# Kernel tuning notes

Measured on AMD Instinct MI355X. Metric: run time of the kernel, lower is better.

Reference implementation:

```python
import jax, jax.numpy as jnp
import numpy as np

EMBED_DIM = 1024
NUM_HEADS = 16
HEAD_DIM = EMBED_DIM // NUM_HEADS
B, S = 2, 2048


def setup_inputs() -> dict:
    key = jax.random.key(0)
    ks = jax.random.split(key, 11)
    scale = 1.0 / np.sqrt(EMBED_DIM)
    inp = {
        "q": jax.random.normal(ks[0], (B, S, EMBED_DIM), jnp.float32),
        "k": jax.random.normal(ks[1], (B, S, EMBED_DIM), jnp.float32),
        "v": jax.random.normal(ks[2], (B, S, EMBED_DIM), jnp.float32),
        "Wq": jax.random.normal(ks[3], (EMBED_DIM, EMBED_DIM), jnp.float32) * scale,
        "bq": jnp.zeros((EMBED_DIM,), jnp.float32),
        "Wk": jax.random.normal(ks[4], (EMBED_DIM, EMBED_DIM), jnp.float32) * scale,
        "bk": jnp.zeros((EMBED_DIM,), jnp.float32),
        "Wv": jax.random.normal(ks[5], (EMBED_DIM, EMBED_DIM), jnp.float32) * scale,
        "bv": jnp.zeros((EMBED_DIM,), jnp.float32),
        "Wo": jax.random.normal(ks[6], (EMBED_DIM, EMBED_DIM), jnp.float32) * scale,
        "bo": jnp.zeros((EMBED_DIM,), jnp.float32),
    }
    return inp


def _split_heads(x):
    # [B, S, E] -> [B, H, S, D]
    b, s, _ = x.shape
    return x.reshape(b, s, NUM_HEADS, HEAD_DIM).transpose(0, 2, 1, 3)


def reference(q, k, v, Wq, bq, Wk, bk, Wv, bv, Wo, bo):
    query = _split_heads(q @ Wq + bq)  # [B,H,S,D]
    key_ = _split_heads(k @ Wk + bk)
    value = _split_heads(v @ Wv + bv)
    # scaled dot-product attention (scale by sqrt(head_dim), as in source)
    logits = jnp.einsum("bhqd,bhkd->bhqk", query, key_) / jnp.sqrt(
        jnp.asarray(HEAD_DIM, jnp.float32)
    )
    weights = jax.nn.softmax(logits, axis=-1)
    attn = jnp.einsum("bhqk,bhkd->bhqd", weights, value)  # [B,H,S,D]
    concat = attn.transpose(0, 2, 1, 3).reshape(q.shape[0], -1, EMBED_DIM)
    return concat @ Wo + bo
```

## Files before the change

kernel.cpp:

```cpp
#include <hip/hip_runtime.h>
#include <hip/hip_bf16.h>
#include <math.h>


typedef short bf16x8 __attribute__((ext_vector_type(8)));
typedef short bf16x4 __attribute__((ext_vector_type(4)));
typedef float f32x4 __attribute__((ext_vector_type(4)));
typedef unsigned short u16;
typedef unsigned int u32;

#if defined(__HIP_DEVICE_COMPILE__) && __has_builtin(__builtin_amdgcn_mfma_f32_16x16x16_bf16)
#define MFMA16(a, b, c) __builtin_amdgcn_mfma_f32_16x16x16_bf16(a, b, c, 0, 0, 0)
#else
#define MFMA16(a, b, c) __builtin_amdgcn_mfma_f32_16x16x16bf16_1k(a, b, c, 0, 0, 0)
#endif

#define QSCALE 0.18033688011112042f

__device__ __forceinline__ u16 f2b(float f) {
  union { float f; unsigned u; } v; v.f = f;
  unsigned r = v.u + 0x7FFF + ((v.u >> 16) & 1);
  return (u16)(r >> 16);
}

__device__ __forceinline__ void glds16(const u16* g, u16* l) {
  __builtin_amdgcn_global_load_lds(
      (const __attribute__((address_space(1))) u32*)g,
      (__attribute__((address_space(3))) u32*)l, 16, 0, 0);
}

__global__ void prep(const float* __restrict__ q, const float* __restrict__ k,
                     const float* __restrict__ v, u16* __restrict__ qo,
                     u16* __restrict__ ko, u16* __restrict__ vo,
                     const float* __restrict__ W0, const float* __restrict__ W1,
                     const float* __restrict__ W2, const float* __restrict__ W3,
                     u16* __restrict__ T0, u16* __restrict__ T1,
                     u16* __restrict__ T2, u16* __restrict__ T3) {
  __shared__ float tile[64][65];
  int z = blockIdx.y;
  if (z < 3) {
    const float* in = z == 0 ? q : (z == 1 ? k : v);
    u16* out = z == 0 ? qo : (z == 1 ? ko : vo);
    int i = (blockIdx.x * 256 + threadIdx.x) * 8;
    float4 a = *(const float4*)(in + i);
    float4 b = *(const float4*)(in + i + 4);
    union { u16 u[8]; uint4 v4; } o;
    o.u[0] = f2b(a.x); o.u[1] = f2b(a.y); o.u[2] = f2b(a.z); o.u[3] = f2b(a.w);
    o.u[4] = f2b(b.x); o.u[5] = f2b(b.y); o.u[6] = f2b(b.z); o.u[7] = f2b(b.w);
    *(uint4*)(out + i) = o.v4;
  } else {
    int bx = blockIdx.x;
    if (bx >= 1024) return;
    int wsel = bx >> 8, tid2 = bx & 255;
    const float* W = wsel == 0 ? W0 : (wsel == 1 ? W1 : (wsel == 2 ? W2 : W3));
    u16* WT = wsel == 0 ? T0 : (wsel == 1 ? T1 : (wsel == 2 ? T2 : T3));
    int k0 = (tid2 >> 4) * 64, n0 = (tid2 & 15) * 64;
    int c = threadIdx.x & 63, r0 = threadIdx.x >> 6;
    #pragma unroll
    for (int i = 0; i < 64; i += 4)
      tile[r0 + i][c] = W[(k0 + r0 + i) * 1024 + n0 + c];
    __syncthreads();
    #pragma unroll
    for (int i = 0; i < 64; i += 4)
      WT[(n0 + r0 + i) * 1024 + k0 + c] = f2b(tile[c][r0 + i]);
  }
}

template<int MODE, int BN>
__device__ __forceinline__ void gemm_core(
    const u16* __restrict__ A, const u16* __restrict__ BT,
    const float* __restrict__ bias, void* __restrict__ out,
    int bx, int by, float scale) {
  constexpr int NT = BN / 64 * 2;
  __shared__ u16 As[128 * 64];
  __shared__ u16 Bs[BN * 64];
  const int tid = threadIdx.x;
  const int w = tid >> 6, lane = tid & 63;
  const int wm = w >> 1, wn = w & 1;
  const int q = lane >> 4, l16 = lane & 15;
  const int m0 = by * 128, n0 = bx * BN;
  const int K = 1024;

  f32x4 acc[4][NT] = {};
  for (int k0 = 0; k0 < K; k0 += 64) {
    __syncthreads();
    #pragma unroll
    for (int p = 0; p < 4; ++p) {
      int c = p * 4 + w;
      int ci = c * 64 + lane;
      int r = ci >> 3, b = ci & 7;
      glds16(A + (m0 + r) * K + k0 + ((b ^ (r & 7)) * 8), As + c * 512);
    }
    #pragma unroll
    for (int p = 0; p < BN / 32; ++p) {
      int c = p * 4 + w;
      int ci = c * 64 + lane;
      int r = ci >> 3, b = ci & 7;
      glds16(BT + (n0 + r) * K + k0 + ((b ^ (r & 7)) * 8), Bs + c * 512);
    }
    __builtin_amdgcn_s_waitcnt(0xF70);
    __syncthreads();
    #pragma unroll
    for (int ks = 0; ks < 2; ++ks) {
      bf16x8 af[4], bf[NT];
      #pragma unroll
      for (int mt = 0; mt < 4; ++mt) {
        int row = wm * 64 + mt * 16 + l16;
        af[mt] = *(const bf16x8*)(As + row * 64 + (((ks * 4 + q) ^ (row & 7)) * 8));
      }
      #pragma unroll
      for (int nt = 0; nt < NT; ++nt) {
        int row = wn * (BN / 2) + nt * 16 + l16;
        bf[nt] = *(const bf16x8*)(Bs + row * 64 + (((ks * 4 + q) ^ (row & 7)) * 8));
      }
      #pragma unroll
      for (int mt = 0; mt < 4; ++mt)
        #pragma unroll
        for (int nt = 0; nt < NT; ++nt)
          acc[mt][nt] = __builtin_amdgcn_mfma_f32_16x16x32_bf16(af[mt], bf[nt], acc[mt][nt], 0, 0, 0);
    }
  }
  #pragma unroll
  for (int mt = 0; mt < 4; ++mt)
    #pragma unroll
    for (int nt = 0; nt < NT; ++nt) {
      int col = n0 + wn * (BN / 2) + nt * 16 + l16;
      float bcol = bias[col];
      if (MODE == 2) {
        int rbase = m0 + wm * 64 + mt * 16 + q * 4;
        int b = rbase >> 11, s0 = rbase & 2047;
        int h = col >> 6, d = col & 63;
        union { u16 u[4]; uint2 v; } o;
        #pragma unroll
        for (int reg = 0; reg < 4; ++reg)
          o.u[reg] = f2b(acc[mt][nt][reg] + bcol);
        *(uint2*)((u16*)out + (((b << 4) + h) * 64 + d) * 2048 + s0) = o.v;
      } else {
        #pragma unroll
        for (int reg = 0; reg < 4; ++reg) {
          int row = m0 + wm * 64 + mt * 16 + q * 4 + reg;
          float val = (acc[mt][nt][reg] + bcol) * scale;
          if (MODE == 0) {
            int b = row >> 11, s = row & 2047, h = col >> 6, d = col & 63;
            ((u16*)out)[(((b << 4) + h) * 2048 + s) * 64 + d] = f2b(val);
          } else {
            ((float*)out)[row * 1024 + col] = val;
          }
        }
      }
    }
}

__global__ __launch_bounds__(256) void gemm_qkv(
    const u16* qb, const u16* kb, const u16* vb,
    const u16* WqT, const u16* WkT, const u16* WvT,
    const float* bq, const float* bk, const float* bv,
    u16* Qh, u16* Kh, u16* VhT) {
  int z = blockIdx.z;
  if (z == 0)      gemm_core<0, 128>(qb, WqT, bq, Qh,  blockIdx.x, blockIdx.y, QSCALE);
  else if (z == 1) gemm_core<0, 128>(kb, WkT, bk, Kh,  blockIdx.x, blockIdx.y, 1.0f);
  else             gemm_core<2, 128>(vb, WvT, bv, VhT, blockIdx.x, blockIdx.y, 1.0f);
}

__global__ __launch_bounds__(256) void gemm_out(
    const u16* A, const u16* BT, const float* bias, float* out) {
  gemm_core<1, 64>(A, BT, bias, out, blockIdx.x, blockIdx.y, 1.0f);
}

__global__ __launch_bounds__(512, 4) void flash_attn(
    const u16* __restrict__ Qh, const u16* __restrict__ Kh,
    const u16* __restrict__ VTh, u16* __restrict__ Oo) {
  __shared__ __align__(16) u16 smem[32768];
  const int tid = threadIdx.x, w = tid >> 6, lane = tid & 63;
  const int g = w >> 2, w4 = w & 3;
  const int q = lane >> 4, l16 = lane & 15;
  const int bh = blockIdx.x & 31, qt = blockIdx.x >> 5;
  const u16* Qp = Qh + (bh * 2048 + qt * 128) * 64;
  const u16* Kp = Kh + (bh * 2048 + g * 1024) * 64;
  const u16* Vp = VTh + bh * 64 * 2048 + g * 1024;
  u16* Ksg = smem + g * 8192;
  u16* Vtg = smem + 16384 + g * 8192;

  bf16x8 aq[2][2];
  #pragma unroll
  for (int rb = 0; rb < 2; ++rb)
    #pragma unroll
    for (int ks = 0; ks < 2; ++ks)
      aq[rb][ks] = *(const bf16x8*)(Qp + (w4 * 32 + rb * 16 + l16) * 64 + ks * 32 + q * 8);

  const int sr = (lane & 7) ^ (lane >> 3);
  auto stage = [&](int kt, int buf) {
    #pragma unroll
    for (int p = 0; p < 2; ++p) {
      int c = p * 4 + w4;
      int r = c * 8 + (lane >> 3);
      glds16(Kp + (kt * 64 + r) * 64 + sr * 8, Ksg + buf * 4096 + c * 512);
    }
    #pragma unroll
    for (int p = 0; p < 2; ++p) {
      int c = p * 4 + w4;
      int r = c * 8 + (lane >> 3);
      glds16(Vp + r * 2048 + kt * 64 + sr * 8, Vtg + buf * 4096 + c * 512);
    }
  };
  stage(0, 0);

  f32x4 oacc[4][2] = {};
  float lacc[2] = {0.f, 0.f};

  for (int kt = 0; kt < 16; ++kt) {
    const int buf = kt & 1;
    __builtin_amdgcn_s_waitcnt(0xF70);
    __syncthreads();
    if (kt + 1 < 16) stage(kt + 1, buf ^ 1);

    const u16* KsT = Ksg + buf * 4096;
    const u16* VtT = Vtg + buf * 4096;

    f32x4 st[2][4] = {};
    __builtin_amdgcn_s_setprio(1);
    #pragma unroll
    for (int ks = 0; ks < 2; ++ks) {
      bf16x8 bk[4];
      #pragma unroll
      for (int nt = 0; nt < 4; ++nt) {
        int row = nt * 16 + l16;
        bk[nt] = *(const bf16x8*)(KsT + row * 64 + (((ks * 4 + q) ^ (l16 & 7)) * 8));
      }
      #pragma unroll
      for (int rb = 0; rb < 2; ++rb)
        #pragma unroll
        for (int nt = 0; nt < 4; ++nt)
          st[rb][nt] = __builtin_amdgcn_mfma_f32_16x16x32_bf16(bk[nt], aq[rb][ks], st[rb][nt], 0, 0, 0);
    }
    __builtin_amdgcn_s_setprio(0);

    #pragma unroll
    for (int rb = 0; rb < 2; ++rb)
      #pragma unroll
      for (int nt = 0; nt < 4; ++nt)
        #pragma unroll
        for (int reg = 0; reg < 4; ++reg) {
          float p = __builtin_amdgcn_exp2f(st[rb][nt][reg]);
          lacc[rb] += p;
          st[rb][nt][reg] = p;
        }

    __builtin_amdgcn_s_setprio(1);
    #pragma unroll
    for (int kb = 0; kb < 4; ++kb) {
      bf16x4 pf[2];
      #pragma unroll
      for (int rb = 0; rb < 2; ++rb) {
        union { u32 u[2]; bf16x4 v; } pk;
        pk.u[0] = __builtin_amdgcn_perm(__float_as_uint(st[rb][kb][1]),
                                        __float_as_uint(st[rb][kb][0]), 0x07060302u);
        pk.u[1] = __builtin_amdgcn_perm(__float_as_uint(st[rb][kb][3]),
                                        __float_as_uint(st[rb][kb][2]), 0x07060302u);
        pf[rb] = pk.v;
      }
      #pragma unroll
      for (int ntd = 0; ntd < 4; ++ntd) {
        int row = ntd * 16 + l16;
        int c = kb * 2 + (q >> 1);
        bf16x4 vf = *(const bf16x4*)(VtT + row * 64 + ((c ^ (l16 & 7)) * 8) + (q & 1) * 4);
        #pragma unroll
        for (int rb = 0; rb < 2; ++rb)
          oacc[ntd][rb] = MFMA16(vf, pf[rb], oacc[ntd][rb]);
      }
    }
    __builtin_amdgcn_s_setprio(0);
  }

  __syncthreads();
  float* Ocmb = (float*)smem;
  float* Lcmb = (float*)(smem + 18432);
  const int idx = w4 * 64 + lane;
  if (g == 1) {
    #pragma unroll
    for (int ntd = 0; ntd < 4; ++ntd)
      #pragma unroll
      for (int rb = 0; rb < 2; ++rb)
        *(f32x4*)(Ocmb + idx * 36 + ntd * 8 + rb * 4) = oacc[ntd][rb];
    Lcmb[idx * 2 + 0] = lacc[0];
    Lcmb[idx * 2 + 1] = lacc[1];
  }
  __syncthreads();
  if (g == 0) {
    #pragma unroll
    for (int ntd = 0; ntd < 4; ++ntd)
      #pragma unroll
      for (int rb = 0; rb < 2; ++rb)
        oacc[ntd][rb] += *(const f32x4*)(Ocmb + idx * 36 + ntd * 8 + rb * 4);
    lacc[0] += Lcmb[idx * 2 + 0];
    lacc[1] += Lcmb[idx * 2 + 1];

    const int b = bh >> 4, h = bh & 15;
    #pragma unroll
    for (int rb = 0; rb < 2; ++rb) {
      float s = lacc[rb];
      s += __shfl_xor(s, 16);
      s += __shfl_xor(s, 32);
      float rl = 0.998046875f / s;
      int row = b * 2048 + qt * 128 + w4 * 32 + rb * 16 + l16;
      #pragma unroll
      for (int ntd = 0; ntd < 4; ++ntd) {
        union { u16 u[4]; uint2 v; } o;
        #pragma unroll
        for (int reg = 0; reg < 4; ++reg)
          o.u[reg] = f2b(oacc[ntd][rb][reg] * rl);
        *(uint2*)(Oo + row * 1024 + h * 64 + ntd * 16 + q * 4) = o.v;
      }
    }
  }
}

extern "C" void kernel_launch(void* const* d_in, const int* in_sizes, int n_in,
                              void* d_out, int out_size, void* d_ws, size_t ws_size,
                              hipStream_t stream) {
  const float* q  = (const float*)d_in[0];
  const float* k  = (const float*)d_in[1];
  const float* v  = (const float*)d_in[2];
  const float* Wq = (const float*)d_in[3];
  const float* bq = (const float*)d_in[4];
  const float* Wk = (const float*)d_in[5];
  const float* bk = (const float*)d_in[6];
  const float* Wv = (const float*)d_in[7];
  const float* bv = (const float*)d_in[8];
  const float* Wo = (const float*)d_in[9];
  const float* bo = (const float*)d_in[10];

  char* ws = (char*)d_ws;
  const size_t MB = 1024 * 1024;
  u16* qb  = (u16*)(ws);
  u16* kb  = (u16*)(ws + 8 * MB);
  u16* vb  = (u16*)(ws + 16 * MB);
  u16* WqT = (u16*)(ws + 24 * MB);
  u16* WkT = (u16*)(ws + 26 * MB);
  u16* WvT = (u16*)(ws + 28 * MB);
  u16* WoT = (u16*)(ws + 30 * MB);
  u16* Qh  = (u16*)(ws + 32 * MB);
  u16* Kh  = (u16*)(ws + 40 * MB);
  u16* VhT = (u16*)(ws + 48 * MB);
  u16* Ao  = (u16*)(ws + 56 * MB);

  prep<<<dim3(2048, 4), 256, 0, stream>>>(q, k, v, qb, kb, vb,
                                          Wq, Wk, Wv, Wo, WqT, WkT, WvT, WoT);
  gemm_qkv<<<dim3(8, 32, 3), 256, 0, stream>>>(qb, kb, vb, WqT, WkT, WvT,
                                               bq, bk, bv, Qh, Kh, VhT);
  flash_attn<<<512, 512, 0, stream>>>(Qh, Kh, VhT, Ao);
  gemm_out<<<dim3(16, 32), 256, 0, stream>>>(Ao, WoT, bo, (float*)d_out);
}
```

Before: 227.6 us.

## Drop split-KV in flash attention, use 4-wave blocks, widen output GEMM tile

The flash attention kernel stops splitting the key range across two wave groups. Each 256-thread block now walks all 32 key tiles itself, which removes the shared-memory cross-group reduction and its extra barriers, and halves LDS use so more blocks can fit per CU. The exp/row-sum loop is rewritten as a tree-style partial sum, and the output GEMM moves to a 128-wide tile with half as many blocks. In exchange, each wave has a longer serial loop with less parallelism per block, and the output GEMM grid is smaller.

Result: slower. 291.8 us (+28.2%).

```diff
diff --git a/kernel.cpp b/kernel.cpp
--- a/kernel.cpp
+++ b/kernel.cpp
@@ -164,43 +164,42 @@
 
 __global__ __launch_bounds__(256) void gemm_out(
     const u16* A, const u16* BT, const float* bias, float* out) {
-  gemm_core<1, 64>(A, BT, bias, out, blockIdx.x, blockIdx.y, 1.0f);
-}
-
-__global__ __launch_bounds__(512, 4) void flash_attn(
+  gemm_core<1, 128>(A, BT, bias, out, blockIdx.x, blockIdx.y, 1.0f);
+}
+
+__global__ __launch_bounds__(256, 5) void flash_attn(
     const u16* __restrict__ Qh, const u16* __restrict__ Kh,
     const u16* __restrict__ VTh, u16* __restrict__ Oo) {
-  __shared__ __align__(16) u16 smem[32768];
+  __shared__ __align__(16) u16 Ks[2][4096];
+  __shared__ __align__(16) u16 Vt[2][4096];
+
   const int tid = threadIdx.x, w = tid >> 6, lane = tid & 63;
-  const int g = w >> 2, w4 = w & 3;
   const int q = lane >> 4, l16 = lane & 15;
   const int bh = blockIdx.x & 31, qt = blockIdx.x >> 5;
   const u16* Qp = Qh + (bh * 2048 + qt * 128) * 64;
-  const u16* Kp = Kh + (bh * 2048 + g * 1024) * 64;
-  const u16* Vp = VTh + bh * 64 * 2048 + g * 1024;
-  u16* Ksg = smem + g * 8192;
-  u16* Vtg = smem + 16384 + g * 8192;
+  const u16* Kp = Kh + bh * 2048 * 64;
+  const u16* Vp = VTh + bh * 64 * 2048;
 
   bf16x8 aq[2][2];
   #pragma unroll
   for (int rb = 0; rb < 2; ++rb)
     #pragma unroll
     for (int ks = 0; ks < 2; ++ks)
-      aq[rb][ks] = *(const bf16x8*)(Qp + (w4 * 32 + rb * 16 + l16) * 64 + ks * 32 + q * 8);
+      aq[rb][ks] = *(const bf16x8*)(Qp + (w * 32 + rb * 16 + l16) * 64 + ks * 32 + q * 8);
 
   const int sr = (lane & 7) ^ (lane >> 3);
   auto stage = [&](int kt, int buf) {
     #pragma unroll
     for (int p = 0; p < 2; ++p) {
-      int c = p * 4 + w4;
+      int c = p * 4 + w;
       int r = c * 8 + (lane >> 3);
-      glds16(Kp + (kt * 64 + r) * 64 + sr * 8, Ksg + buf * 4096 + c * 512);
+      glds16(Kp + (kt * 64 + r) * 64 + sr * 8, &Ks[buf][c * 512]);
     }
     #pragma unroll
     for (int p = 0; p < 2; ++p) {
-      int c = p * 4 + w4;
+      int c = p * 4 + w;
       int r = c * 8 + (lane >> 3);
-      glds16(Vp + r * 2048 + kt * 64 + sr * 8, Vtg + buf * 4096 + c * 512);
+      glds16(Vp + r * 2048 + kt * 64 + sr * 8, &Vt[buf][c * 512]);
     }
   };
   stage(0, 0);
@@ -208,14 +207,14 @@
   f32x4 oacc[4][2] = {};
   float lacc[2] = {0.f, 0.f};
 
-  for (int kt = 0; kt < 16; ++kt) {
+  for (int kt = 0; kt < 32; ++kt) {
     const int buf = kt & 1;
     __builtin_amdgcn_s_waitcnt(0xF70);
     __syncthreads();
-    if (kt + 1 < 16) stage(kt + 1, buf ^ 1);
-
-    const u16* KsT = Ksg + buf * 4096;
-    const u16* VtT = Vtg + buf * 4096;
+    if (kt + 1 < 32) stage(kt + 1, buf ^ 1);
+
+    const u16* KsT = Ks[buf];
+    const u16* VtT = Vt[buf];
 
     f32x4 st[2][4] = {};
     __builtin_amdgcn_s_setprio(1);
@@ -236,15 +235,20 @@
     __builtin_amdgcn_s_setprio(0);
 
     #pragma unroll
-    for (int rb = 0; rb < 2; ++rb)
-      #pragma unroll
-      for (int nt = 0; nt < 4; ++nt)
-        #pragma unroll
-        for (int reg = 0; reg < 4; ++reg) {
-          float p = __builtin_amdgcn_exp2f(st[rb][nt][reg]);
-          lacc[rb] += p;
-          st[rb][nt][reg] = p;
-        }
+    for (int rb = 0; rb < 2; ++rb) {
+      float part[4];
+      #pragma unroll
+      for (int nt = 0; nt < 4; ++nt) {
+        float p0 = __builtin_amdgcn_exp2f(st[rb][nt][0]);
+        float p1 = __builtin_amdgcn_exp2f(st[rb][nt][1]);
+        float p2 = __builtin_amdgcn_exp2f(st[rb][nt][2]);
+        float p3 = __builtin_amdgcn_exp2f(st[rb][nt][3]);
+        st[rb][nt][0] = p0; st[rb][nt][1] = p1;
+        st[rb][nt][2] = p2; st[rb][nt][3] = p3;
+        part[nt] = (p0 + p1) + (p2 + p3);
+      }
+      lacc[rb] += (part[0] + part[1]) + (part[2] + part[3]);
+    }
 
     __builtin_amdgcn_s_setprio(1);
     #pragma unroll
@@ -272,45 +276,26 @@
     __builtin_amdgcn_s_setprio(0);
   }
 
-  __syncthreads();
-  float* Ocmb = (float*)smem;
-  float* Lcmb = (float*)(smem + 18432);
-  const int idx = w4 * 64 + lane;
-  if (g == 1) {
-    #pragma unroll
-    for (int ntd = 0; ntd < 4; ++ntd)
-      #pragma unroll
-      for (int rb = 0; rb < 2; ++rb)
-        *(f32x4*)(Ocmb + idx * 36 + ntd * 8 + rb * 4) = oacc[ntd][rb];
-    Lcmb[idx * 2 + 0] = lacc[0];
-    Lcmb[idx * 2 + 1] = lacc[1];
-  }
-  __syncthreads();
-  if (g == 0) {
-    #pragma unroll
-    for (int ntd = 0; ntd < 4; ++ntd)
-      #pragma unroll
-      for (int rb = 0; rb < 2; ++rb)
-        oacc[ntd][rb] += *(const f32x4*)(Ocmb + idx * 36 + ntd * 8 + rb * 4);
-    lacc[0] += Lcmb[idx * 2 + 0];
-    lacc[1] += Lcmb[idx * 2 + 1];
-
-    const int b = bh >> 4, h = bh & 15;
-    #pragma unroll
-    for (int rb = 0; rb < 2; ++rb) {
-      float s = lacc[rb];
-      s += __shfl_xor(s, 16);
-      s += __shfl_xor(s, 32);
-      float rl = 0.998046875f / s;
-      int row = b * 2048 + qt * 128 + w4 * 32 + rb * 16 + l16;
-      #pragma unroll
-      for (int ntd = 0; ntd < 4; ++ntd) {
-        union { u16 u[4]; uint2 v; } o;
-        #pragma unroll
-        for (int reg = 0; reg < 4; ++reg)
-          o.u[reg] = f2b(oacc[ntd][rb][reg] * rl);
-        *(uint2*)(Oo + row * 1024 + h * 64 + ntd * 16 + q * 4) = o.v;
-      }
+  float rl[2];
+  #pragma unroll
+  for (int rb = 0; rb < 2; ++rb) {
+    float s = lacc[rb];
+    s += __shfl_xor(s, 16);
+    s += __shfl_xor(s, 32);
+    rl[rb] = 0.998046875f / s;
+  }
+
+  const int b = bh >> 4, h = bh & 15;
+  #pragma unroll
+  for (int rb = 0; rb < 2; ++rb) {
+    int row = b * 2048 + qt * 128 + w * 32 + rb * 16 + l16;
+    #pragma unroll
+    for (int ntd = 0; ntd < 4; ++ntd) {
+      union { u16 u[4]; uint2 v; } o;
+      #pragma unroll
+      for (int reg = 0; reg < 4; ++reg)
+        o.u[reg] = f2b(oacc[ntd][rb][reg] * rl[rb]);
+      *(uint2*)(Oo + row * 1024 + h * 64 + ntd * 16 + q * 4) = o.v;
     }
   }
 }
@@ -348,6 +333,6 @@
                                           Wq, Wk, Wv, Wo, WqT, WkT, WvT, WoT);
   gemm_qkv<<<dim3(8, 32, 3), 256, 0, stream>>>(qb, kb, vb, WqT, WkT, WvT,
                                                bq, bk, bv, Qh, Kh, VhT);
-  flash_attn<<<512, 512, 0, stream>>>(Qh, Kh, VhT, Ao);
-  gemm_out<<<dim3(16, 32), 256, 0, stream>>>(Ao, WoT, bo, (float*)d_out);
-}
+  flash_attn<<<512, 256, 0, stream>>>(Qh, Kh, VhT, Ao);
+  gemm_out<<<dim3(8, 32), 256, 0, stream>>>(Ao, WoT, bo, (float*)d_out);
+}
```

## Fuse fp32-to-bf16 input conversion into QKV projection GEMM tile loads

Applied to the files above, without the earlier changes.

Removes the separate pass that converted q/k/v activations to bf16, and has the QKV GEMM load fp32 tiles directly into LDS with a swizzled layout. Each fragment is converted to bf16 with packed convert instructions just before the MFMAs. This avoids writing and re-reading the bf16 copies of the activations, at the cost of double LDS for the A tile, twice the global bytes per A tile load, and extra conversion instructions in the inner loop. The weight transpose becomes its own kernel.

New measurement: 265.2 us. 1.16x slower.

```diff
diff --git a/kernel.cpp b/kernel.cpp
--- a/kernel.cpp
+++ b/kernel.cpp
@@ -23,57 +23,53 @@
   return (u16)(r >> 16);
 }
 
+__device__ __forceinline__ u32 cvtpk2(float a, float b) {
+  u32 r;
+#if defined(__HIP_DEVICE_COMPILE__)
+  asm("v_cvt_pk_bf16_f32 %0, %1, %2" : "=v"(r) : "v"(a), "v"(b));
+#else
+  r = ((u32)f2b(b) << 16) | f2b(a);
+#endif
+  return r;
+}
+
 __device__ __forceinline__ void glds16(const u16* g, u16* l) {
   __builtin_amdgcn_global_load_lds(
       (const __attribute__((address_space(1))) u32*)g,
       (__attribute__((address_space(3))) u32*)l, 16, 0, 0);
 }
-
-__global__ void prep(const float* __restrict__ q, const float* __restrict__ k,
-                     const float* __restrict__ v, u16* __restrict__ qo,
-                     u16* __restrict__ ko, u16* __restrict__ vo,
-                     const float* __restrict__ W0, const float* __restrict__ W1,
-                     const float* __restrict__ W2, const float* __restrict__ W3,
-                     u16* __restrict__ T0, u16* __restrict__ T1,
-                     u16* __restrict__ T2, u16* __restrict__ T3) {
+__device__ __forceinline__ void glds16f(const float* g, float* l) {
+  __builtin_amdgcn_global_load_lds(
+      (const __attribute__((address_space(1))) u32*)g,
+      (__attribute__((address_space(3))) u32*)l, 16, 0, 0);
+}
+
+__global__ void transpose_w4(const float* __restrict__ W0, const float* __restrict__ W1,
+                             const float* __restrict__ W2, const float* __restrict__ W3,
+                             u16* __restrict__ T0, u16* __restrict__ T1,
+                             u16* __restrict__ T2, u16* __restrict__ T3) {
+  const float* W = blockIdx.z == 0 ? W0 : (blockIdx.z == 1 ? W1 : (blockIdx.z == 2 ? W2 : W3));
+  u16* WT = blockIdx.z == 0 ? T0 : (blockIdx.z == 1 ? T1 : (blockIdx.z == 2 ? T2 : T3));
   __shared__ float tile[64][65];
-  int z = blockIdx.y;
-  if (z < 3) {
-    const float* in = z == 0 ? q : (z == 1 ? k : v);
-    u16* out = z == 0 ? qo : (z == 1 ? ko : vo);
-    int i = (blockIdx.x * 256 + threadIdx.x) * 8;
-    float4 a = *(const float4*)(in + i);
-    float4 b = *(const float4*)(in + i + 4);
-    union { u16 u[8]; uint4 v4; } o;
-    o.u[0] = f2b(a.x); o.u[1] = f2b(a.y); o.u[2] = f2b(a.z); o.u[3] = f2b(a.w);
-    o.u[4] = f2b(b.x); o.u[5] = f2b(b.y); o.u[6] = f2b(b.z); o.u[7] = f2b(b.w);
-    *(uint4*)(out + i) = o.v4;
-  } else {
-    int bx = blockIdx.x;
-    if (bx >= 1024) return;
-    int wsel = bx >> 8, tid2 = bx & 255;
-    const float* W = wsel == 0 ? W0 : (wsel == 1 ? W1 : (wsel == 2 ? W2 : W3));
-    u16* WT = wsel == 0 ? T0 : (wsel == 1 ? T1 : (wsel == 2 ? T2 : T3));
-    int k0 = (tid2 >> 4) * 64, n0 = (tid2 & 15) * 64;
-    int c = threadIdx.x & 63, r0 = threadIdx.x >> 6;
-    #pragma unroll
-    for (int i = 0; i < 64; i += 4)
-      tile[r0 + i][c] = W[(k0 + r0 + i) * 1024 + n0 + c];
-    __syncthreads();
-    #pragma unroll
-    for (int i = 0; i < 64; i += 4)
-      WT[(n0 + r0 + i) * 1024 + k0 + c] = f2b(tile[c][r0 + i]);
-  }
-}
-
-template<int MODE, int BN>
+  int k0 = blockIdx.y * 64, n0 = blockIdx.x * 64;
+  int c = threadIdx.x & 63, r0 = threadIdx.x >> 6;
+  #pragma unroll
+  for (int i = 0; i < 64; i += 4)
+    tile[r0 + i][c] = W[(k0 + r0 + i) * 1024 + n0 + c];
+  __syncthreads();
+  #pragma unroll
+  for (int i = 0; i < 64; i += 4)
+    WT[(n0 + r0 + i) * 1024 + k0 + c] = f2b(tile[c][r0 + i]);
+}
+
+template<int MODE, int BN, int AF32>
 __device__ __forceinline__ void gemm_core(
-    const u16* __restrict__ A, const u16* __restrict__ BT,
+    const void* __restrict__ Av, const u16* __restrict__ BT,
     const float* __restrict__ bias, void* __restrict__ out,
     int bx, int by, float scale) {
   constexpr int NT = BN / 64 * 2;
-  __shared__ u16 As[128 * 64];
-  __shared__ u16 Bs[BN * 64];
+  __shared__ __align__(16) u16 As[AF32 ? 128 * 128 : 128 * 64];
+  __shared__ __align__(16) u16 Bs[BN * 64];
   const int tid = threadIdx.x;
   const int w = tid >> 6, lane = tid & 63;
   const int wm = w >> 1, wn = w & 1;
@@ -84,12 +80,25 @@
   f32x4 acc[4][NT] = {};
   for (int k0 = 0; k0 < K; k0 += 64) {
     __syncthreads();
-    #pragma unroll
-    for (int p = 0; p < 4; ++p) {
-      int c = p * 4 + w;
-      int ci = c * 64 + lane;
-      int r = ci >> 3, b = ci & 7;
-      glds16(A + (m0 + r) * K + k0 + ((b ^ (r & 7)) * 8), As + c * 512);
+    if (AF32) {
+      const float* Af = (const float*)Av;
+      #pragma unroll
+      for (int p = 0; p < 8; ++p) {
+        int c = p * 4 + w;
+        int r = c * 4 + (lane >> 4);
+        int b = lane & 15;
+        glds16f(Af + (m0 + r) * K + k0 + ((b ^ ((r & 7) << 1)) * 4),
+                (float*)As + c * 256);
+      }
+    } else {
+      const u16* Ab = (const u16*)Av;
+      #pragma unroll
+      for (int p = 0; p < 4; ++p) {
+        int c = p * 4 + w;
+        int ci = c * 64 + lane;
+        int r = ci >> 3, b = ci & 7;
+        glds16(Ab + (m0 + r) * K + k0 + ((b ^ (r & 7)) * 8), As + c * 512);
+      }
     }
     #pragma unroll
     for (int p = 0; p < BN / 32; ++p) {
@@ -106,7 +115,19 @@
       #pragma unroll
       for (int mt = 0; mt < 4; ++mt) {
         int row = wm * 64 + mt * 16 + l16;
-        af[mt] = *(const bf16x8*)(As + row * 64 + (((ks * 4 + q) ^ (row & 7)) * 8));
+        if (AF32) {
+          const float* Asf = (const float*)As;
+          int cc = (ks * 8 + q * 2) ^ ((row & 7) << 1);
+          const float* ap = Asf + row * 64 + cc * 4;
+          f32x4 lo = *(const f32x4*)ap;
+          f32x4 hi = *(const f32x4*)(ap + 4);
+          union { u32 u[4]; bf16x8 v; } cv;
+          cv.u[0] = cvtpk2(lo[0], lo[1]); cv.u[1] = cvtpk2(lo[2], lo[3]);
+          cv.u[2] = cvtpk2(hi[0], hi[1]); cv.u[3] = cvtpk2(hi[2], hi[3]);
+          af[mt] = cv.v;
+        } else {
+          af[mt] = *(const bf16x8*)(As + row * 64 + (((ks * 4 + q) ^ (row & 7)) * 8));
+        }
       }
       #pragma unroll
       for (int nt = 0; nt < NT; ++nt) {
@@ -152,19 +173,19 @@
 }
 
 __global__ __launch_bounds__(256) void gemm_qkv(
-    const u16* qb, const u16* kb, const u16* vb,
+    const float* q, const float* k, const float* v,
     const u16* WqT, const u16* WkT, const u16* WvT,
     const float* bq, const float* bk, const float* bv,
     u16* Qh, u16* Kh, u16* VhT) {
   int z = blockIdx.z;
-  if (z == 0)      gemm_core<0, 128>(qb, WqT, bq, Qh,  blockIdx.x, blockIdx.y, QSCALE);
-  else if (z == 1) gemm_core<0, 128>(kb, WkT, bk, Kh,  blockIdx.x, blockIdx.y, 1.0f);
-  else             gemm_core<2, 128>(vb, WvT, bv, VhT, blockIdx.x, blockIdx.y, 1.0f);
+  if (z == 0)      gemm_core<0, 128, 1>(q, WqT, bq, Qh,  blockIdx.x, blockIdx.y, QSCALE);
+  else if (z == 1) gemm_core<0, 128, 1>(k, WkT, bk, Kh,  blockIdx.x, blockIdx.y, 1.0f);
+  else             gemm_core<2, 128, 1>(v, WvT, bv, VhT, blockIdx.x, blockIdx.y, 1.0f);
 }
 
 __global__ __launch_bounds__(256) void gemm_out(
     const u16* A, const u16* BT, const float* bias, float* out) {
-  gemm_core<1, 64>(A, BT, bias, out, blockIdx.x, blockIdx.y, 1.0f);
+  gemm_core<1, 64, 0>(A, BT, bias, out, blockIdx.x, blockIdx.y, 1.0f);
 }
 
 __global__ __launch_bounds__(512, 4) void flash_attn(
@@ -332,9 +353,6 @@
 
   char* ws = (char*)d_ws;
   const size_t MB = 1024 * 1024;
-  u16* qb  = (u16*)(ws);
-  u16* kb  = (u16*)(ws + 8 * MB);
-  u16* vb  = (u16*)(ws + 16 * MB);
   u16* WqT = (u16*)(ws + 24 * MB);
   u16* WkT = (u16*)(ws + 26 * MB);
   u16* WvT = (u16*)(ws + 28 * MB);
@@ -344,9 +362,8 @@
   u16* VhT = (u16*)(ws + 48 * MB);
   u16* Ao  = (u16*)(ws + 56 * MB);
 
-  prep<<<dim3(2048, 4), 256, 0, stream>>>(q, k, v, qb, kb, vb,
-                                          Wq, Wk, Wv, Wo, WqT, WkT, WvT, WoT);
-  gemm_qkv<<<dim3(8, 32, 3), 256, 0, stream>>>(qb, kb, vb, WqT, WkT, WvT,
+  transpose_w4<<<dim3(16, 16, 4), 256, 0, stream>>>(Wq, Wk, Wv, Wo, WqT, WkT, WvT, WoT);
+  gemm_qkv<<<dim3(8, 32, 3), 256, 0, stream>>>(q, k, v, WqT, WkT, WvT,
                                                bq, bk, bv, Qh, Kh, VhT);
   flash_attn<<<512, 512, 0, stream>>>(Qh, Kh, VhT, Ao);
   gemm_out<<<dim3(16, 32), 256, 0, stream>>>(Ao, WoT, bo, (float*)d_out);
```
